# Optimization experiments

Hardware: AMD Instinct MI355X
Metric: run time of the kernel (lower is better)

The kernel has to match this reference:

```python
import jax, jax.numpy as jnp
import numpy as np

EMBED_DIM = 1024
NUM_HEADS = 16
HEAD_DIM = EMBED_DIM // NUM_HEADS
EXPANSION = 4
EPS = 1e-5


def setup_inputs() -> dict:
    key = jax.random.key(0)
    ks = jax.random.split(key, 8)
    D, F = EMBED_DIM, EMBED_DIM * EXPANSION
    s = lambda d: 1.0 / np.sqrt(d)
    return {
        "x": jax.random.normal(ks[0], (8, 1024, D), jnp.float32),
        "qkv_w": jax.random.normal(ks[1], (D, 3 * D), jnp.float32) * s(D),
        "qkv_b": jnp.zeros((3 * D,), jnp.float32),
        "out_w": jax.random.normal(ks[2], (D, D), jnp.float32) * s(D),
        "out_b": jnp.zeros((D,), jnp.float32),
        "ffn_w1": jax.random.normal(ks[3], (D, F), jnp.float32) * s(D),
        "ffn_b1": jnp.zeros((F,), jnp.float32),
        "ffn_w2": jax.random.normal(ks[4], (F, D), jnp.float32) * s(F),
        "ffn_b2": jnp.zeros((D,), jnp.float32),
        "ln1_g": jnp.ones((D,), jnp.float32),
        "ln1_b": jnp.zeros((D,), jnp.float32),
        "ln2_g": jnp.ones((D,), jnp.float32),
        "ln2_b": jnp.zeros((D,), jnp.float32),
    }


def _layernorm(x, g, b):
    mu = jnp.mean(x, axis=-1, keepdims=True)
    var = jnp.mean(jnp.square(x - mu), axis=-1, keepdims=True)
    return (x - mu) * jax.lax.rsqrt(var + EPS) * g + b


def reference(x, qkv_w, qkv_b, out_w, out_b, ffn_w1, ffn_b1, ffn_w2, ffn_b2,
              ln1_g, ln1_b, ln2_g, ln2_b):
    B, N, D = x.shape
    H, Hd = NUM_HEADS, HEAD_DIM
    scale = Hd ** -0.5

    residual = x
    h = _layernorm(x, ln1_g, ln1_b)
    qkv = h @ qkv_w + qkv_b                      # [B, N, 3D]
    q, k, v = jnp.split(qkv, 3, axis=-1)
    # [B, N, D] -> [B, H, N, Hd]
    reshape = lambda t: t.reshape(B, N, H, Hd).transpose(0, 2, 1, 3)
    q, k, v = reshape(q), reshape(k), reshape(v)

    attn = jnp.einsum("bhnd,bhmd->bhnm", q, k) * scale
    attn = jax.nn.softmax(attn, axis=-1)
    o = jnp.einsum("bhnm,bhmd->bhnd", attn, v)   # [B, H, N, Hd]
    o = o.transpose(0, 2, 1, 3).reshape(B, N, D)
    o = o @ out_w + out_b
    x = residual + o

    residual = x
    h = _layernorm(x, ln2_g, ln2_b)
    h = jax.nn.gelu(h @ ffn_w1 + ffn_b1, approximate=False) @ ffn_w2 + ffn_b2
    return residual + h
```

## Files before the change

### kernel.cpp

```cpp
#include <hip/hip_runtime.h>
#include <hip/hip_bf16.h>


typedef float f32x4 __attribute__((ext_vector_type(4)));
typedef float f32x16 __attribute__((ext_vector_type(16)));
typedef short bf16x8 __attribute__((ext_vector_type(8)));

#define DEV __device__ __forceinline__

DEV f32x4 mfma16(bf16x8 a, bf16x8 b, f32x4 c) {
    return __builtin_amdgcn_mfma_f32_16x16x32_bf16(a, b, c, 0, 0, 0);
}

DEV f32x16 mfma32(bf16x8 a, bf16x8 b, f32x16 c) {
    return __builtin_amdgcn_mfma_f32_32x32x16_bf16(a, b, c, 0, 0, 0);
}

DEV ushort f2bf(float f) {
    union { float f; unsigned u; } v; v.f = f;
    unsigned r = v.u + 0x7FFFu + ((v.u >> 16) & 1u);
    return (ushort)(r >> 16);
}

DEV unsigned cvtpk(float lo, float hi) {
    unsigned r;
    asm("v_cvt_pk_bf16_f32 %0, %1, %2" : "=v"(r) : "v"(lo), "v"(hi));
    return r;
}

DEV void gload_lds16(const void* g, void* l) {
    __builtin_amdgcn_global_load_lds(
        (const __attribute__((address_space(1))) void*)g,
        (__attribute__((address_space(3))) void*)l, 16, 0, 0);
}

template <int N> DEV void vmwait() {
    asm volatile("s_waitcnt vmcnt(%0)" :: "n"(N) : "memory");
}
DEV void lgkm0() {
    asm volatile("s_waitcnt lgkmcnt(0)" ::: "memory");
}

__global__ __launch_bounds__(256) void transpose_w(
    const float* __restrict__ src, ushort* __restrict__ dst, int K, int N)
{
    __shared__ float tile[32][33];
    const int n0 = blockIdx.x * 32, k0 = blockIdx.y * 32;
    const int tx = threadIdx.x, ty = threadIdx.y;
#pragma unroll
    for (int i = 0; i < 32; i += 8)
        tile[ty + i][tx] = src[(size_t)(k0 + ty + i) * N + n0 + tx];
    __syncthreads();
#pragma unroll
    for (int i = 0; i < 32; i += 8)
        dst[(size_t)(n0 + ty + i) * K + k0 + tx] = f2bf(tile[tx][ty + i]);
}

__global__ __launch_bounds__(256) void transpose_v(
    const ushort* __restrict__ qkvb, ushort* __restrict__ vt)
{
    __shared__ ushort tile[32][33];
    const int b = blockIdx.z >> 4, h = blockIdx.z & 15;
    const int n0 = blockIdx.x * 32, d0 = blockIdx.y * 32;
    const int tx = threadIdx.x, ty = threadIdx.y;
#pragma unroll
    for (int i = 0; i < 32; i += 8)
        tile[ty + i][tx] =
            qkvb[(size_t)(b * 1024 + n0 + ty + i) * 3072 + 2048 + h * 64 + d0 + tx];
    __syncthreads();
#pragma unroll
    for (int i = 0; i < 32; i += 8)
        vt[((size_t)(b * 16 + h) * 64 + d0 + ty + i) * 1024 + n0 + tx] = tile[tx][ty + i];
}

__global__ __launch_bounds__(256) void ln_bf16(
    const float* __restrict__ x, const float* __restrict__ gw,
    const float* __restrict__ bw, ushort* __restrict__ out)
{
    const int row = blockIdx.x;
    const int t = threadIdx.x;
    const float4 v = ((const float4*)(x + (size_t)row * 1024))[t];
    float s  = v.x + v.y + v.z + v.w;
    float s2 = v.x * v.x + v.y * v.y + v.z * v.z + v.w * v.w;
#pragma unroll
    for (int off = 32; off; off >>= 1) {
        s  += __shfl_xor(s, off);
        s2 += __shfl_xor(s2, off);
    }
    __shared__ float red[16];
    const int wave = t >> 6, lane = t & 63;
    if (lane == 0) { red[wave] = s; red[8 + wave] = s2; }
    __syncthreads();
    s  = red[0] + red[1] + red[2] + red[3];
    s2 = red[8] + red[9] + red[10] + red[11];
    const float mean = s * (1.0f / 1024.0f);
    const float var  = s2 * (1.0f / 1024.0f) - mean * mean;
    const float rstd = rsqrtf(var + 1e-5f);
    const float4 gv = ((const float4*)gw)[t];
    const float4 bv = ((const float4*)bw)[t];
    ushort4 o;
    o.x = f2bf((v.x - mean) * rstd * gv.x + bv.x);
    o.y = f2bf((v.y - mean) * rstd * gv.y + bv.y);
    o.z = f2bf((v.z - mean) * rstd * gv.z + bv.z);
    o.w = f2bf((v.w - mean) * rstd * gv.w + bv.w);
    ((ushort4*)out)[(size_t)row * 256 + t] = o;
}

template <int BM, int BN, int WM_, int WN_, int EPI>
__global__ __launch_bounds__(512, 2) void gemm_pipe(
    const ushort* __restrict__ A, const ushort* __restrict__ BT,
    const float* __restrict__ bias, const float* __restrict__ res,
    void* __restrict__ out, int M, int N, int K)
{
    constexpr int BK = 64;
    constexpr int MR = BM / WM_ / 16;
    constexpr int NR = BN / WN_ / 16;
    constexpr int MQ = MR / 2, NQ = NR / 2;
    constexpr int VT = (BM + BN) / 64;
    constexpr int ABYTES = BM * BK * 2;
    constexpr int BBYTES = BN * BK * 2;

    extern __shared__ __align__(16) char smem[];
#define ASB(buf) (smem + (buf) * ABYTES)
#define BSB(buf) (smem + 2 * ABYTES + (buf) * BBYTES)

    const int tid = threadIdx.x;
    const int wave = tid >> 6, lane = tid & 63;
    const int g = lane >> 4, lr = lane & 15;
    const int wr = wave / WN_, wc = wave % WN_;
    const int akey = (lr & 7) << 4;

    const int gx = gridDim.x;
    const int nwg = gx * gridDim.y;
    int id = blockIdx.y * gx + blockIdx.x;
    id = (id & 7) * (nwg >> 3) + (id >> 3);
    const int m0 = (id / gx) * BM, n0 = (id % gx) * BN;

    const int trow = tid >> 3;
    const int tblk = (tid & 7) ^ (trow & 7);
    const ushort* pA = A  + (size_t)(m0 + trow) * K + tblk * 8;
    const ushort* pB = BT + (size_t)(n0 + trow) * K + tblk * 8;
    const int woff = wave * 1024;

#define STAGE_TILE(buf, kt) do { \
    _Pragma("unroll") for (int i = 0; i < BM / 64; ++i) \
        gload_lds16(pA + ((size_t)(i * 64)) * K + (size_t)(kt) * 64, \
                    ASB(buf) + i * 8192 + woff); \
    _Pragma("unroll") for (int i = 0; i < BN / 64; ++i) \
        gload_lds16(pB + ((size_t)(i * 64)) * K + (size_t)(kt) * 64, \
                    BSB(buf) + i * 8192 + woff); \
} while (0)

    bf16x8 afE[MR][2], bfE[NR][2], afO[MR][2], bfO[NR][2];
    f32x4 acc[MR][NR] = {};

#define READ_FRAGS(AF, BF, buf) do { \
    _Pragma("unroll") for (int mi = 0; mi < MR; ++mi) { \
        const char* rb_ = ASB(buf) + (mi / MQ) * (BM / 2) * 128 \
                        + (wr * (MQ * 16) + (mi % MQ) * 16 + lr) * 128; \
        _Pragma("unroll") for (int kk = 0; kk < 2; ++kk) \
            AF[mi][kk] = *(const bf16x8*)(rb_ + ((kk * 64 + g * 16) ^ akey)); \
    } \
    _Pragma("unroll") for (int ni = 0; ni < NR; ++ni) { \
        const char* rb_ = BSB(buf) + (ni / NQ) * (BN / 2) * 128 \
                        + (wc * (NQ * 16) + (ni % NQ) * 16 + lr) * 128; \
        _Pragma("unroll") for (int kk = 0; kk < 2; ++kk) \
            BF[ni][kk] = *(const bf16x8*)(rb_ + ((kk * 64 + g * 16) ^ akey)); \
    } \
} while (0)

#define MFMA_ALL(AF, BF) do { \
    __builtin_amdgcn_s_setprio(1); \
    _Pragma("unroll") for (int mi = 0; mi < MR; ++mi) \
    _Pragma("unroll") for (int ni = 0; ni < NR; ++ni) \
    _Pragma("unroll") for (int kk = 0; kk < 2; ++kk) \
        acc[mi][ni] = mfma16(AF[mi][kk], BF[ni][kk], acc[mi][ni]); \
    __builtin_amdgcn_s_setprio(0); \
} while (0)

#define ITER(kt, CA, CB, PA, PB, BUFC) do { \
    lgkm0();                                    \
    __builtin_amdgcn_s_barrier();               \
    if ((kt) + 2 < NT) STAGE_TILE(BUFC, (kt) + 2); \
    if ((kt) + 1 < NT) { \
        if ((kt) + 2 < NT) vmwait<VT>(); else vmwait<0>(); \
        __builtin_amdgcn_s_barrier();           \
        READ_FRAGS(PA, PB, 1 - (BUFC)); \
    } \
    MFMA_ALL(CA, CB); \
} while (0)

    const int NT = K >> 6;

    STAGE_TILE(0, 0);
    STAGE_TILE(1, 1);
    vmwait<VT>();
    __builtin_amdgcn_s_barrier();
    READ_FRAGS(afE, bfE, 0);

    for (int kt = 0; kt < NT; kt += 2) {
        ITER(kt,     afE, bfE, afO, bfO, 0);
        ITER(kt + 1, afO, bfO, afE, bfE, 1);
    }

#pragma unroll
    for (int mi = 0; mi < MR; ++mi) {
        const int row0 = m0 + (mi / MQ) * (BM / 2) + wr * (MQ * 16) + (mi % MQ) * 16 + 4 * g;
#pragma unroll
        for (int ni = 0; ni < NR; ++ni) {
            const int col = n0 + (ni / NQ) * (BN / 2) + wc * (NQ * 16) + (ni % NQ) * 16 + lr;
            const float bv = bias[col];
#pragma unroll
            for (int r = 0; r < 4; ++r) {
                float v = acc[mi][ni][r] + bv;
                const size_t idx = (size_t)(row0 + r) * N + col;
                if constexpr (EPI == 1) {
                    ((float*)out)[idx] = v + res[idx];
                } else if constexpr (EPI == 2) {
                    v = 0.5f * v * (1.0f + erff(v * 0.70710678118654752f));
                    ((ushort*)out)[idx] = f2bf(v);
                } else {
                    ((ushort*)out)[idx] = f2bf(v);
                }
            }
        }
    }
#undef STAGE_TILE
#undef READ_FRAGS
#undef MFMA_ALL
#undef ITER
#undef ASB
#undef BSB
}

__global__ __launch_bounds__(256) void attn_kernel(
    const ushort* __restrict__ qkv, const ushort* __restrict__ vtb,
    ushort* __restrict__ o)
{
    __shared__ __align__(16) ushort Ks[64 * 64];
    __shared__ __align__(16) ushort Vt[64 * 64];

    const int tid = threadIdx.x;
    const int wave = tid >> 6, lane = tid & 63;
    const int lq = lane & 31;
    const int hi = lane >> 5;
    const int l7 = lane & 7;

    const int hwid = blockIdx.x;
    const int logical = (hwid & 7) * 128 + (hwid >> 3);
    const int bh = logical >> 3, qt = logical & 7;
    const int b = bh >> 4, head = bh & 15;
    const int q0 = qt * 128 + wave * 32;

    const size_t base  = (size_t)b * 1024 * 3072;
    const size_t vbase = (size_t)bh * 64 * 1024;

    union BF8 { bf16x8 v; ushort u[8]; unsigned w[4]; };

    BF8 qf[4];
    {
        const ushort* qrow = qkv + base + (size_t)(q0 + lq) * 3072 + head * 64;
#pragma unroll
        for (int s = 0; s < 4; ++s) {
            *(ushort4*)&qf[s].u[0] = *(const ushort4*)(qrow + 16 * s + 4 * hi);
            *(ushort4*)&qf[s].u[4] = *(const ushort4*)(qrow + 16 * s + 8 + 4 * hi);
        }
    }

    const int sr = tid >> 3, sc = tid & 7;
    const int swz = (sc ^ (sr & 7)) << 3;
    const ushort* kg0 = qkv + base + (size_t)sr * 3072 + 1024 + head * 64 + sc * 8;
    const ushort* kg1 = kg0 + (size_t)32 * 3072;
    const ushort* vg0 = vtb + vbase + (size_t)sr * 1024 + sc * 8;
    const ushort* vg1 = vg0 + (size_t)32 * 1024;
    ushort* ksw0 = Ks + sr * 64 + swz;
    ushort* ksw1 = Ks + (sr + 32) * 64 + swz;
    ushort* vsw0 = Vt + sr * 64 + swz;
    ushort* vsw1 = Vt + (sr + 32) * 64 + swz;

    float m_st = -1e30f, l_st = 0.f;
    f32x16 oacc[2] = {};

    constexpr float SCL = 0.18033688011112042f;

    for (int kt = 0; kt < 16; ++kt) {
        const int n0 = kt * 64;
        __syncthreads();
        *(bf16x8*)ksw0 = *(const bf16x8*)(kg0 + (size_t)n0 * 3072);
        *(bf16x8*)ksw1 = *(const bf16x8*)(kg1 + (size_t)n0 * 3072);
        *(bf16x8*)vsw0 = *(const bf16x8*)(vg0 + n0);
        *(bf16x8*)vsw1 = *(const bf16x8*)(vg1 + n0);
        __syncthreads();

        f32x16 sacc[2];
#pragma unroll
        for (int kb = 0; kb < 2; ++kb) {
            f32x16 a = {};
            const ushort* krow = Ks + (kb * 32 + lq) * 64;
#pragma unroll
            for (int s = 0; s < 4; ++s) {
                BF8 kf;
                *(ushort4*)&kf.u[0] = *(const ushort4*)(krow + (((2 * s)     ^ l7) << 3) + 4 * hi);
                *(ushort4*)&kf.u[4] = *(const ushort4*)(krow + (((2 * s + 1) ^ l7) << 3) + 4 * hi);
                a = mfma32(kf.v, qf[s].v, a);
            }
            sacc[kb] = a;
        }

        float mloc = -1e30f;
#pragma unroll
        for (int kb = 0; kb < 2; ++kb)
#pragma unroll
            for (int r = 0; r < 16; ++r)
                mloc = fmaxf(mloc, sacc[kb][r]);
        mloc = fmaxf(mloc, __shfl_xor(mloc, 32));
        const float mnew = fmaxf(m_st, mloc * SCL);
        const float resc = exp2f(m_st - mnew);
        m_st = mnew;

        float psum = 0.f;
#pragma unroll
        for (int kb = 0; kb < 2; ++kb)
#pragma unroll
            for (int r = 0; r < 16; ++r) {
                const float pe = exp2f(fmaf(sacc[kb][r], SCL, -mnew));
                sacc[kb][r] = pe;
                psum += pe;
            }
        psum += __shfl_xor(psum, 32);
        l_st = l_st * resc + psum;
#pragma unroll
        for (int nb = 0; nb < 2; ++nb)
#pragma unroll
            for (int r = 0; r < 16; ++r)
                oacc[nb][r] *= resc;

#pragma unroll
        for (int kb = 0; kb < 2; ++kb) {
            BF8 pf[2];
#pragma unroll
            for (int t = 0; t < 2; ++t)
#pragma unroll
                for (int w = 0; w < 4; ++w)
                    pf[t].w[w] = cvtpk(sacc[kb][8 * t + 2 * w], sacc[kb][8 * t + 2 * w + 1]);
#pragma unroll
            for (int nb = 0; nb < 2; ++nb) {
                const ushort* vrow = Vt + (nb * 32 + lq) * 64;
#pragma unroll
                for (int t = 0; t < 2; ++t) {
                    BF8 vf;
                    const int blk = 4 * kb + 2 * t;
                    *(ushort4*)&vf.u[0] = *(const ushort4*)(vrow + ((blk       ^ l7) << 3) + 4 * hi);
                    *(ushort4*)&vf.u[4] = *(const ushort4*)(vrow + (((blk + 1) ^ l7) << 3) + 4 * hi);
                    oacc[nb] = mfma32(vf.v, pf[t].v, oacc[nb]);
                }
            }
        }
    }

    const float inv = 1.0f / l_st;
    ushort* orow = o + (size_t)(b * 1024 + q0 + lq) * 1024 + head * 64;
#pragma unroll
    for (int nb = 0; nb < 2; ++nb)
#pragma unroll
        for (int u = 0; u < 4; ++u) {
            uint2 wv;
            wv.x = cvtpk(oacc[nb][4 * u] * inv,     oacc[nb][4 * u + 1] * inv);
            wv.y = cvtpk(oacc[nb][4 * u + 2] * inv, oacc[nb][4 * u + 3] * inv);
            *(uint2*)(orow + nb * 32 + 8 * u + 4 * hi) = wv;
        }
}

extern "C" void kernel_launch(void* const* d_in, const int* in_sizes, int n_in,
                              void* d_out, int out_size, void* d_ws, size_t ws_size,
                              hipStream_t stream)
{
    const float* x      = (const float*)d_in[0];
    const float* qkv_w  = (const float*)d_in[1];
    const float* qkv_b  = (const float*)d_in[2];
    const float* out_w  = (const float*)d_in[3];
    const float* out_b  = (const float*)d_in[4];
    const float* ffn_w1 = (const float*)d_in[5];
    const float* ffn_b1 = (const float*)d_in[6];
    const float* ffn_w2 = (const float*)d_in[7];
    const float* ffn_b2 = (const float*)d_in[8];
    const float* ln1_g  = (const float*)d_in[9];
    const float* ln1_b  = (const float*)d_in[10];
    const float* ln2_g  = (const float*)d_in[11];
    const float* ln2_b  = (const float*)d_in[12];

    constexpr size_t MB = 1u << 20;
    char* ws = (char*)d_ws;
    ushort* wt_qkv = (ushort*)(ws + 0 * MB);
    ushort* wt_out = (ushort*)(ws + 6 * MB);
    ushort* wt_f1  = (ushort*)(ws + 8 * MB);
    ushort* wt_f2  = (ushort*)(ws + 16 * MB);
    float*  x1     = (float*) (ws + 24 * MB);
    ushort* vtb    = (ushort*)(ws + 24 * MB);
    ushort* hbuf   = (ushort*)(ws + 56 * MB);
    ushort* qkvb   = (ushort*)(ws + 72 * MB);
    ushort* obuf   = (ushort*)(ws + 120 * MB);
    ushort* gbuf   = (ushort*)(ws + 72 * MB);

    const dim3 tb(32, 8);
    transpose_w<<<dim3(3072 / 32, 1024 / 32), tb, 0, stream>>>(qkv_w,  wt_qkv, 1024, 3072);
    transpose_w<<<dim3(1024 / 32, 1024 / 32), tb, 0, stream>>>(out_w,  wt_out, 1024, 1024);
    transpose_w<<<dim3(4096 / 32, 1024 / 32), tb, 0, stream>>>(ffn_w1, wt_f1,  1024, 4096);
    transpose_w<<<dim3(1024 / 32, 4096 / 32), tb, 0, stream>>>(ffn_w2, wt_f2,  4096, 1024);

    ln_bf16<<<8192, 256, 0, stream>>>(x, ln1_g, ln1_b, hbuf);

    constexpr int LDS_PIPE = (128 + 256) * 64 * 2 * 2;

    gemm_pipe<128, 256, 2, 4, 0><<<dim3(12, 64), 512, LDS_PIPE, stream>>>(
        hbuf, wt_qkv, qkv_b, nullptr, qkvb, 8192, 3072, 1024);

    transpose_v<<<dim3(32, 2, 128), tb, 0, stream>>>(qkvb, vtb);

    attn_kernel<<<1024, 256, 0, stream>>>(qkvb, vtb, obuf);

    gemm_pipe<256, 128, 4, 2, 1><<<dim3(8, 32), 512, LDS_PIPE, stream>>>(
        obuf, wt_out, out_b, x, x1, 8192, 1024, 1024);

    ln_bf16<<<8192, 256, 0, stream>>>(x1, ln2_g, ln2_b, hbuf);

    gemm_pipe<128, 256, 2, 4, 2><<<dim3(16, 64), 512, LDS_PIPE, stream>>>(
        hbuf, wt_f1, ffn_b1, nullptr, gbuf, 8192, 4096, 1024);

    gemm_pipe<256, 128, 4, 2, 1><<<dim3(8, 32), 512, LDS_PIPE, stream>>>(
        gbuf, wt_f2, ffn_b2, x1, (float*)d_out, 8192, 1024, 4096);
}
```

Baseline: 395.1 us.

## Restructure GEMM into four-phase half-tile pipeline, enlarge tiles, approximate GELU

The GEMM main loop is split into four phases. Each phase loads a quarter of the A fragments, issues half-tile global-to-LDS stages for the next k-tiles, and runs the MFMAs for that quarter, so copies and math interleave more finely and fewer fragment registers are live. The QKV and FFN1 GEMMs move to 256x256 tiles to raise data reuse. The exact erf GELU is replaced by a tanh-style sigmoid approximation, which is cheaper but changes numerics slightly.

```diff
diff --git a/kernel.cpp b/kernel.cpp
--- a/kernel.cpp
+++ b/kernel.cpp
@@ -107,7 +107,7 @@
 }
 
 template <int BM, int BN, int WM_, int WN_, int EPI>
-__global__ __launch_bounds__(512, 2) void gemm_pipe(
+__global__ __launch_bounds__(512, 2) void gemm4p(
     const ushort* __restrict__ A, const ushort* __restrict__ BT,
     const float* __restrict__ bias, const float* __restrict__ res,
     void* __restrict__ out, int M, int N, int K)
@@ -115,14 +115,17 @@
     constexpr int BK = 64;
     constexpr int MR = BM / WM_ / 16;
     constexpr int NR = BN / WN_ / 16;
-    constexpr int MQ = MR / 2, NQ = NR / 2;
-    constexpr int VT = (BM + BN) / 64;
+    constexpr int MH = MR / 2;
+    constexpr int CM = MH / 2;
+    constexpr int LA = (BM / 2) / 64;
+    constexpr int LB = (BN / 2) / 64;
+    constexpr int VMN = LA + LB;
     constexpr int ABYTES = BM * BK * 2;
     constexpr int BBYTES = BN * BK * 2;
 
     extern __shared__ __align__(16) char smem[];
-#define ASB(buf) (smem + (buf) * ABYTES)
-#define BSB(buf) (smem + 2 * ABYTES + (buf) * BBYTES)
+#define ASB(b) (smem + (b) * ABYTES)
+#define BSB(b) (smem + 2 * ABYTES + (b) * BBYTES)
 
     const int tid = threadIdx.x;
     const int wave = tid >> 6, lane = tid & 63;
@@ -142,73 +145,79 @@
     const ushort* pB = BT + (size_t)(n0 + trow) * K + tblk * 8;
     const int woff = wave * 1024;
 
-#define STAGE_TILE(buf, kt) do { \
-    _Pragma("unroll") for (int i = 0; i < BM / 64; ++i) \
-        gload_lds16(pA + ((size_t)(i * 64)) * K + (size_t)(kt) * 64, \
-                    ASB(buf) + i * 8192 + woff); \
-    _Pragma("unroll") for (int i = 0; i < BN / 64; ++i) \
-        gload_lds16(pB + ((size_t)(i * 64)) * K + (size_t)(kt) * 64, \
-                    BSB(buf) + i * 8192 + woff); \
+#define STAGE_A(b, h, kt) do { \
+    _Pragma("unroll") for (int i = 0; i < LA; ++i) \
+        gload_lds16(pA + ((size_t)((h) * (BM / 2) + i * 64)) * K + (size_t)(kt) * 64, \
+                    ASB(b) + (h) * (BM / 2) * 128 + i * 8192 + woff); \
 } while (0)
-
-    bf16x8 afE[MR][2], bfE[NR][2], afO[MR][2], bfO[NR][2];
+#define STAGE_B(b, h, kt) do { \
+    _Pragma("unroll") for (int i = 0; i < LB; ++i) \
+        gload_lds16(pB + ((size_t)((h) * (BN / 2) + i * 64)) * K + (size_t)(kt) * 64, \
+                    BSB(b) + (h) * (BN / 2) * 128 + i * 8192 + woff); \
+} while (0)
+
+    bf16x8 af[CM][2], bfr[NR][2];
     f32x4 acc[MR][NR] = {};
 
-#define READ_FRAGS(AF, BF, buf) do { \
-    _Pragma("unroll") for (int mi = 0; mi < MR; ++mi) { \
-        const char* rb_ = ASB(buf) + (mi / MQ) * (BM / 2) * 128 \
-                        + (wr * (MQ * 16) + (mi % MQ) * 16 + lr) * 128; \
-        _Pragma("unroll") for (int kk = 0; kk < 2; ++kk) \
-            AF[mi][kk] = *(const bf16x8*)(rb_ + ((kk * 64 + g * 16) ^ akey)); \
-    } \
-    _Pragma("unroll") for (int ni = 0; ni < NR; ++ni) { \
-        const char* rb_ = BSB(buf) + (ni / NQ) * (BN / 2) * 128 \
-                        + (wc * (NQ * 16) + (ni % NQ) * 16 + lr) * 128; \
-        _Pragma("unroll") for (int kk = 0; kk < 2; ++kk) \
-            BF[ni][kk] = *(const bf16x8*)(rb_ + ((kk * 64 + g * 16) ^ akey)); \
-    } \
+#define LOAD_A(b, h, cj) do { \
+    const char* rb_ = ASB(b) + ((h) * (BM / 2) + wr * ((BM / 2) / WM_) \
+                               + (cj) * CM * 16 + lr) * 128; \
+    _Pragma("unroll") for (int cm = 0; cm < CM; ++cm) \
+    _Pragma("unroll") for (int kk = 0; kk < 2; ++kk) \
+        af[cm][kk] = *(const bf16x8*)(rb_ + cm * 2048 + ((kk * 64 + g * 16) ^ akey)); \
 } while (0)
-
-#define MFMA_ALL(AF, BF) do { \
-    __builtin_amdgcn_s_setprio(1); \
-    _Pragma("unroll") for (int mi = 0; mi < MR; ++mi) \
+#define LOAD_B(b) do { \
+    const char* rb_ = BSB(b) + (wc * (BN / WN_) + lr) * 128; \
     _Pragma("unroll") for (int ni = 0; ni < NR; ++ni) \
     _Pragma("unroll") for (int kk = 0; kk < 2; ++kk) \
-        acc[mi][ni] = mfma16(AF[mi][kk], BF[ni][kk], acc[mi][ni]); \
+        bfr[ni][kk] = *(const bf16x8*)(rb_ + ni * 2048 + ((kk * 64 + g * 16) ^ akey)); \
+} while (0)
+#define MFMA_PH(h, cj) do { \
+    __builtin_amdgcn_s_setprio(1); \
+    _Pragma("unroll") for (int cm = 0; cm < CM; ++cm) \
+    _Pragma("unroll") for (int ni = 0; ni < NR; ++ni) \
+    _Pragma("unroll") for (int kk = 0; kk < 2; ++kk) \
+        acc[(h) * MH + (cj) * CM + cm][ni] = \
+            mfma16(af[cm][kk], bfr[ni][kk], acc[(h) * MH + (cj) * CM + cm][ni]); \
     __builtin_amdgcn_s_setprio(0); \
 } while (0)
 
-#define ITER(kt, CA, CB, PA, PB, BUFC) do { \
-    lgkm0();                                    \
-    __builtin_amdgcn_s_barrier();               \
-    if ((kt) + 2 < NT) STAGE_TILE(BUFC, (kt) + 2); \
-    if ((kt) + 1 < NT) { \
-        if ((kt) + 2 < NT) vmwait<VT>(); else vmwait<0>(); \
-        __builtin_amdgcn_s_barrier();           \
-        READ_FRAGS(PA, PB, 1 - (BUFC)); \
-    } \
-    MFMA_ALL(CA, CB); \
-} while (0)
-
     const int NT = K >> 6;
 
-    STAGE_TILE(0, 0);
-    STAGE_TILE(1, 1);
-    vmwait<VT>();
+    STAGE_A(0, 0, 0); STAGE_A(0, 1, 0); STAGE_B(0, 0, 0); STAGE_B(0, 1, 0);
+    STAGE_B(1, 0, 1);
+    STAGE_A(1, 0, 1);
+    vmwait<VMN>();
     __builtin_amdgcn_s_barrier();
-    READ_FRAGS(afE, bfE, 0);
-
-    for (int kt = 0; kt < NT; kt += 2) {
-        ITER(kt,     afE, bfE, afO, bfO, 0);
-        ITER(kt + 1, afO, bfO, afE, bfE, 1);
+
+    for (int kt = 0; kt < NT; ++kt) {
+        const int b = kt & 1, nb = b ^ 1;
+        LOAD_A(b, 0, 0); LOAD_B(b);
+        if (kt + 1 < NT) STAGE_B(nb, 1, kt + 1);
+        __builtin_amdgcn_s_barrier(); lgkm0();
+        MFMA_PH(0, 0);
+        LOAD_A(b, 0, 1);
+        if (kt + 1 < NT) STAGE_A(nb, 1, kt + 1);
+        __builtin_amdgcn_s_barrier(); lgkm0();
+        MFMA_PH(0, 1);
+        LOAD_A(b, 1, 0);
+        if (kt + 2 < NT) STAGE_B(b, 0, kt + 2);
+        __builtin_amdgcn_s_barrier(); lgkm0();
+        MFMA_PH(1, 0);
+        LOAD_A(b, 1, 1);
+        if (kt + 2 < NT) { STAGE_A(b, 0, kt + 2); vmwait<VMN>(); }
+        else if (kt + 1 < NT) vmwait<0>();
+        __builtin_amdgcn_s_barrier(); lgkm0();
+        MFMA_PH(1, 1);
     }
 
 #pragma unroll
     for (int mi = 0; mi < MR; ++mi) {
-        const int row0 = m0 + (mi / MQ) * (BM / 2) + wr * (MQ * 16) + (mi % MQ) * 16 + 4 * g;
+        const int row0 = m0 + (mi / MH) * (BM / 2) + wr * ((BM / 2) / WM_)
+                       + (mi % MH) * 16 + 4 * g;
 #pragma unroll
         for (int ni = 0; ni < NR; ++ni) {
-            const int col = n0 + (ni / NQ) * (BN / 2) + wc * (NQ * 16) + (ni % NQ) * 16 + lr;
+            const int col = n0 + wc * (BN / WN_) + ni * 16 + lr;
             const float bv = bias[col];
 #pragma unroll
             for (int r = 0; r < 4; ++r) {
@@ -217,18 +226,20 @@
                 if constexpr (EPI == 1) {
                     ((float*)out)[idx] = v + res[idx];
                 } else if constexpr (EPI == 2) {
-                    v = 0.5f * v * (1.0f + erff(v * 0.70710678118654752f));
-                    ((ushort*)out)[idx] = f2bf(v);
+                    const float u = 1.595769122f * v + 0.071354816f * v * v * v;
+                    const float gs = 1.0f / (1.0f + __expf(-u));
+                    ((ushort*)out)[idx] = f2bf(v * gs);
                 } else {
                     ((ushort*)out)[idx] = f2bf(v);
                 }
             }
         }
     }
-#undef STAGE_TILE
-#undef READ_FRAGS
-#undef MFMA_ALL
-#undef ITER
+#undef STAGE_A
+#undef STAGE_B
+#undef LOAD_A
+#undef LOAD_B
+#undef MFMA_PH
 #undef ASB
 #undef BSB
 }
@@ -410,23 +421,24 @@
 
     ln_bf16<<<8192, 256, 0, stream>>>(x, ln1_g, ln1_b, hbuf);
 
-    constexpr int LDS_PIPE = (128 + 256) * 64 * 2 * 2;
-
-    gemm_pipe<128, 256, 2, 4, 0><<<dim3(12, 64), 512, LDS_PIPE, stream>>>(
+    constexpr int LDS_256 = (256 + 256) * 64 * 2 * 2;
+    constexpr int LDS_128 = (256 + 128) * 64 * 2 * 2;
+
+    gemm4p<256, 256, 2, 4, 0><<<dim3(12, 32), 512, LDS_256, stream>>>(
         hbuf, wt_qkv, qkv_b, nullptr, qkvb, 8192, 3072, 1024);
 
     transpose_v<<<dim3(32, 2, 128), tb, 0, stream>>>(qkvb, vtb);
 
     attn_kernel<<<1024, 256, 0, stream>>>(qkvb, vtb, obuf);
 
-    gemm_pipe<256, 128, 4, 2, 1><<<dim3(8, 32), 512, LDS_PIPE, stream>>>(
+    gemm4p<256, 128, 4, 2, 1><<<dim3(8, 32), 512, LDS_128, stream>>>(
         obuf, wt_out, out_b, x, x1, 8192, 1024, 1024);
 
     ln_bf16<<<8192, 256, 0, stream>>>(x1, ln2_g, ln2_b, hbuf);
 
-    gemm_pipe<128, 256, 2, 4, 2><<<dim3(16, 64), 512, LDS_PIPE, stream>>>(
+    gemm4p<256, 256, 2, 4, 2><<<dim3(16, 32), 512, LDS_256, stream>>>(
         hbuf, wt_f1, ffn_b1, nullptr, gbuf, 8192, 4096, 1024);
 
-    gemm_pipe<256, 128, 4, 2, 1><<<dim3(8, 32), 512, LDS_PIPE, stream>>>(
+    gemm4p<256, 128, 4, 2, 1><<<dim3(8, 32), 512, LDS_128, stream>>>(
         gbuf, wt_f2, ffn_b2, x1, (float*)d_out, 8192, 1024, 4096);
 }
```

Result: faster. 352.2 us (-10.9%).
